# Kernel optimization log

Measured on AMD Instinct MI355X. Metric: run time of the kernel, lower is better.

Reference implementation:

```python
import jax, jax.numpy as jnp
import numpy as np
from jax.scipy.linalg import solve_triangular

REG = 1e-6  # reg_covar added to covariance diagonal
LOG2PI = float(np.log(2.0 * np.pi))
RESP_EPS = 10.0 * float(np.finfo(np.float32).eps)


def _log_gauss(X, means, covs):
    # X: [N,D], means: [K,D], covs: [K,D,D] -> per-sample per-component log N(x|mu_k, Sigma_k): [N,K]
    K, D = means.shape
    eye = jnp.eye(D, dtype=X.dtype)
    chol = jnp.linalg.cholesky(covs + REG * eye)                      # [K,D,D]
    diff = X[None, :, :] - means[:, None, :]                          # [K,N,D]
    sol = jax.vmap(lambda L, d: solve_triangular(L, d.T, lower=True))(chol, diff)  # [K,D,N]
    maha = jnp.sum(sol * sol, axis=1)                                 # [K,N]
    logdet = jnp.sum(jnp.log(jnp.diagonal(chol, axis1=1, axis2=2)), axis=1)  # [K] = 0.5*log|Sigma|
    return (-0.5 * (D * LOG2PI + maha) - logdet[:, None]).T           # [N,K]


def _em_step(X, weights, means, covs):
    N, D = X.shape
    # E-step: responsibilities via stable logsumexp
    lp = _log_gauss(X, means, covs) + jnp.log(weights)[None, :]       # [N,K]
    log_norm = jax.scipy.special.logsumexp(lp, axis=1)                # [N]
    resp = jnp.exp(lp - log_norm[:, None])                            # [N,K]
    # M-step (MLE)
    nk = resp.sum(axis=0) + RESP_EPS                                  # [K]
    new_w = nk / N
    new_means = (resp.T @ X) / nk[:, None]                            # [K,D]
    diff = X[None, :, :] - new_means[:, None, :]                      # [K,N,D]
    new_covs = jnp.einsum('kn,knd,kne->kde', resp.T, diff, diff) / nk[:, None, None]
    new_covs = new_covs + REG * jnp.eye(D, dtype=X.dtype)
    return new_w, new_means, new_covs


def reference(X, weights, means, covariances, n_iter):
    # Normalize provided weights (uniform init in the torch module)
    w0 = weights / jnp.sum(weights)

    def step(carry, _):
        w, m, c = carry
        return _em_step(X, w, m, c), None

    (w, m, c), _ = jax.lax.scan(step, (w0, means, covariances), xs=None, length=n_iter)
    # Final per-sample log-likelihood under the fitted mixture (lower bound)
    lp = _log_gauss(X, m, c) + jnp.log(w)[None, :]
    return jax.scipy.special.logsumexp(lp, axis=1)                    # [N]


def setup_inputs() -> dict:
    key = jax.random.key(0)
    kx, km = jax.random.split(key)
    N, D, K = 100000, 32, 16
    X = jax.random.normal(kx, (N, D), dtype=jnp.float32)
    weights = jnp.ones((K,), dtype=jnp.float32) / K
    means = jax.random.normal(km, (K, D), dtype=jnp.float32)
    covariances = jnp.tile(jnp.eye(D, dtype=jnp.float32)[None], (K, 1, 1))
    return {"X": X, "weights": weights, "means": means, "covariances": covariances, "n_iter": 5}
```

## Files before the change

### kernel.cpp

```cpp
#include <hip/hip_runtime.h>
#include <math.h>

#define REGC 1e-6f
#define LOG2PI 1.83787706640934534f
#define RESP_EPS 1.1920929e-6f

#define PART_K 561
#define RS 16

typedef __attribute__((ext_vector_type(8))) short short8;
typedef __attribute__((ext_vector_type(4))) float f32x4;
typedef unsigned short ushort_t;
typedef unsigned int uint_t;

__device__ __forceinline__ ushort_t f2bf(float x) {
    uint_t u = __float_as_uint(x);
    uint_t r = (u + 0x7fffu + ((u >> 16) & 1u)) >> 16;
    return (ushort_t)r;
}
__device__ __forceinline__ float bf2f(ushort_t h) {
    return __uint_as_float(((uint_t)h) << 16);
}
__device__ __forceinline__ f32x4 shx4(f32x4 v, int m) {
    f32x4 r;
#pragma unroll
    for (int i = 0; i < 4; ++i) r[i] = __shfl_xor(v[i], m);
    return r;
}
__device__ __forceinline__ f32x4 sel4(bool s, f32x4 b, f32x4 a) {
    f32x4 r;
#pragma unroll
    for (int i = 0; i < 4; ++i) r[i] = s ? b[i] : a[i];
    return r;
}
__device__ __forceinline__ short8 pack_rx(const float* r8, const short8 bh, float& row) {
    uint_t u[8];
#pragma unroll
    for (int jj = 0; jj < 8; ++jj) {
        float av = r8[jj] * bf2f((ushort_t)bh[jj]);
        row += av;
        u[jj] = __float_as_uint(av) + 0x8000u;
    }
    short8 out;
    uint_t* o = (uint_t*)&out;
    o[0] = __builtin_amdgcn_perm(u[1], u[0], 0x07060302);
    o[1] = __builtin_amdgcn_perm(u[3], u[2], 0x07060302);
    o[2] = __builtin_amdgcn_perm(u[5], u[4], 0x07060302);
    o[3] = __builtin_amdgcn_perm(u[7], u[6], 0x07060302);
    return out;
}

__global__ __launch_bounds__(256) void gmm_xsplit(const float* __restrict__ X,
                                                  ushort_t* __restrict__ Xh,
                                                  ushort_t* __restrict__ Xl,
                                                  ushort_t* __restrict__ XTH,
                                                  int N) {
    int chunk = blockIdx.x;
    int t = threadIdx.x;
    __shared__ float xsh[32][33];
    int s = t >> 3, q = t & 7;
    int n = chunk * 32 + s;
    float4 v = make_float4(0.f, 0.f, 0.f, 0.f);
    if (n < N) v = ((const float4*)(X + (size_t)n * 32))[q];
    float vv[4] = { v.x, v.y, v.z, v.w };
    xsh[s][q * 4 + 0] = v.x; xsh[s][q * 4 + 1] = v.y;
    xsh[s][q * 4 + 2] = v.z; xsh[s][q * 4 + 3] = v.w;
    if (n < N) {
        ushort_t h[4], l[4];
#pragma unroll
        for (int i = 0; i < 4; ++i) {
            h[i] = f2bf(vv[i]);
            l[i] = f2bf(vv[i] - bf2f(h[i]));
        }
        size_t o = (size_t)n * 32 + q * 4;
        *(uint2*)(Xh + o) = make_uint2((uint_t)h[0] | ((uint_t)h[1] << 16),
                                       (uint_t)h[2] | ((uint_t)h[3] << 16));
        *(uint2*)(Xl + o) = make_uint2((uint_t)l[0] | ((uint_t)l[1] << 16),
                                       (uint_t)l[2] | ((uint_t)l[3] << 16));
    }
    __syncthreads();
    int di = t >> 7;
    int lane = (t >> 1) & 63;
    int jj0 = (t & 1) * 4;
    int c = lane & 15, quad = lane >> 4;
    int d = di * 16 + c;
    ushort_t fh[4];
#pragma unroll
    for (int i = 0; i < 4; ++i) fh[i] = f2bf(xsh[quad * 8 + jj0 + i][d]);
    size_t fo = ((size_t)(chunk * 2 + di) * 64 + lane) * 8 + jj0;
    *(uint2*)(XTH + fo) = make_uint2((uint_t)fh[0] | ((uint_t)fh[1] << 16),
                                     (uint_t)fh[2] | ((uint_t)fh[3] << 16));
}

__global__ __launch_bounds__(64) void gmm_prep0(const float* __restrict__ w,
                                                const float* __restrict__ mu,
                                                const float* __restrict__ cov,
                                                ushort_t* __restrict__ Wh,
                                                ushort_t* __restrict__ Wl,
                                                float* __restrict__ Bv,
                                                float* __restrict__ Cc) {
    int k = blockIdx.x;
    int t = threadIdx.x;
    __shared__ float L[32][33];
    __shared__ float Ai[32][33];
    const float* cv = cov + (size_t)k * 1024;
    const float* muk = mu + (size_t)k * 32;
#pragma unroll
    for (int rep = 0; rep < 16; ++rep) {
        int idx = rep * 64 + t;
        int i = idx >> 5, j = idx & 31;
        L[i][j] = cv[idx] + (i == j ? REGC : 0.f);
    }
    __syncthreads();
#pragma unroll
    for (int j = 0; j < 32; ++j) {
        float s = L[j][j];
#pragma unroll
        for (int p = 0; p < j; ++p) { float v = L[j][p]; s -= v * v; }
        float dj = sqrtf(s);
        if (t > j && t < 32) {
            float s2 = L[t][j];
#pragma unroll
            for (int p = 0; p < j; ++p) s2 -= L[t][p] * L[j][p];
            L[t][j] = s2 / dj;
        }
        if (t == j) L[j][j] = dj;
        __syncthreads();
    }
    if (t < 32) {
        float ai[32];
#pragma unroll
        for (int r = 0; r < 32; ++r) {
            float s = (r == t) ? 1.f : 0.f;
#pragma unroll
            for (int p = 0; p < r; ++p) s -= L[r][p] * ai[p];
            ai[r] = s / L[r][r];
        }
#pragma unroll
        for (int r = 0; r < 32; ++r) Ai[r][t] = ai[r];
    }
    __syncthreads();
#pragma unroll
    for (int rep = 0; rep < 16; ++rep) {
        int idx = rep * 64 + t;
        int i = idx >> 5, j = idx & 31;
        float v = Ai[i][j];
        ushort_t h = f2bf(v);
        Wh[(size_t)(k * 32 + i) * 32 + j] = h;
        Wl[(size_t)(k * 32 + i) * 32 + j] = f2bf(v - bf2f(h));
    }
    if (t < 32) {
        float s = 0.f;
#pragma unroll
        for (int j = 0; j < 32; ++j) s += Ai[t][j] * muk[j];
        Bv[k * 32 + t] = s;
    }
    float wsum = 0.f;
#pragma unroll
    for (int i = 0; i < 16; ++i) wsum += w[i];
    float lv = (t < 32) ? logf(L[t & 31][t & 31]) : 0.f;
#pragma unroll
    for (int off = 1; off < 32; off <<= 1) lv += __shfl_xor(lv, off);
    if (t == 0) Cc[k] = logf(w[k] / wsum) - 0.5f * 32.0f * LOG2PI - lv;
}

__global__ __launch_bounds__(512) __attribute__((amdgpu_waves_per_eu(4)))
void gmm_emstep(const ushort_t* __restrict__ Xh, const ushort_t* __restrict__ Xl,
                const ushort_t* __restrict__ XTH,
                const ushort_t* __restrict__ Wh, const ushort_t* __restrict__ Wl,
                const float* __restrict__ Bv, const float* __restrict__ Cc,
                float* __restrict__ part, int N) {
    __shared__ float rsh[16][260];
    int t = threadIdx.x;
    int wave = t >> 6, lane = t & 63;
    int quad = lane >> 4, c = lane & 15;

    int wstart0 = (int)blockIdx.x * 256 + wave * 32;
    bool dup = (wstart0 + 32 > N);
    int wst = dup ? ((N >= 32) ? N - 32 : 0) : wstart0;

    size_t xo0 = (size_t)(wst + c) * 32 + quad * 8;
    size_t xo1 = (size_t)(wst + 16 + c) * 32 + quad * 8;
    short8 ah0 = *(const short8*)(Xh + xo0);
    short8 al0 = *(const short8*)(Xl + xo0);
    short8 ah1 = *(const short8*)(Xh + xo1);
    short8 al1 = *(const short8*)(Xl + xo1);

    {
        f32x4 p0[2], p1[2], p2[2], p3[2], fin[2];
#pragma unroll
        for (int k = 0; k < 16; ++k) {
            size_t w0 = (size_t)(k * 32 + c) * 32 + quad * 8;
            size_t w1 = w0 + 512;
            short8 bh0 = *(const short8*)(Wh + w0);
            short8 bl0 = *(const short8*)(Wl + w0);
            short8 bh1 = *(const short8*)(Wh + w1);
            short8 bl1 = *(const short8*)(Wl + w1);
            float bv0 = Bv[k * 32 + c];
            float bv1 = Bv[k * 32 + 16 + c];
#pragma unroll
            for (int tt = 0; tt < 2; ++tt) {
                short8 ah = tt ? ah1 : ah0;
                short8 al = tt ? al1 : al0;
                f32x4 a0 = {0.f, 0.f, 0.f, 0.f};
                f32x4 a1 = {0.f, 0.f, 0.f, 0.f};
                a0 = __builtin_amdgcn_mfma_f32_16x16x32_bf16(ah, bh0, a0, 0, 0, 0);
                a0 = __builtin_amdgcn_mfma_f32_16x16x32_bf16(ah, bl0, a0, 0, 0, 0);
                a0 = __builtin_amdgcn_mfma_f32_16x16x32_bf16(al, bh0, a0, 0, 0, 0);
                a1 = __builtin_amdgcn_mfma_f32_16x16x32_bf16(ah, bh1, a1, 0, 0, 0);
                a1 = __builtin_amdgcn_mfma_f32_16x16x32_bf16(ah, bl1, a1, 0, 0, 0);
                a1 = __builtin_amdgcn_mfma_f32_16x16x32_bf16(al, bh1, a1, 0, 0, 0);
                f32x4 ms;
#pragma unroll
                for (int r = 0; r < 4; ++r) {
                    float d0 = a0[r] - bv0;
                    float d1 = a1[r] - bv1;
                    ms[r] = fmaf(d0, d0, d1 * d1);
                }
                if ((k & 1) == 0) { p0[tt] = ms; }
                else {
                    f32x4 a = p0[tt] + shx4(p0[tt], 1);
                    f32x4 b = ms + shx4(ms, 1);
                    f32x4 v = sel4((c & 1) != 0, b, a);
                    if ((k & 2) == 0) { p1[tt] = v; }
                    else {
                        a = p1[tt] + shx4(p1[tt], 2); b = v + shx4(v, 2); v = sel4((c & 2) != 0, b, a);
                        if ((k & 4) == 0) { p2[tt] = v; }
                        else {
                            a = p2[tt] + shx4(p2[tt], 4); b = v + shx4(v, 4); v = sel4((c & 4) != 0, b, a);
                            if ((k & 8) == 0) { p3[tt] = v; }
                            else {
                                a = p3[tt] + shx4(p3[tt], 8); b = v + shx4(v, 8);
                                fin[tt] = sel4((c & 8) != 0, b, a);
                            }
                        }
                    }
                }
            }
        }
        float ccv = Cc[c];
#pragma unroll
        for (int tt = 0; tt < 2; ++tt) {
            f32x4 lp;
#pragma unroll
            for (int r = 0; r < 4; ++r) lp[r] = ccv - 0.5f * fin[tt][r];
            f32x4 mx = lp;
#pragma unroll
            for (int off = 1; off < 16; off <<= 1) {
                f32x4 s = shx4(mx, off);
#pragma unroll
                for (int r = 0; r < 4; ++r) mx[r] = fmaxf(mx[r], s[r]);
            }
            f32x4 e;
#pragma unroll
            for (int r = 0; r < 4; ++r) e[r] = __expf(lp[r] - mx[r]);
            f32x4 sm = e;
#pragma unroll
            for (int off = 1; off < 16; off <<= 1) sm = sm + shx4(sm, off);
            f32x4 sv;
#pragma unroll
            for (int r = 0; r < 4; ++r) sv[r] = dup ? 0.f : e[r] / sm[r];
            *(f32x4*)&rsh[c][wave * 32 + tt * 16 + quad * 4] = sv;
        }
    }
    __syncthreads();

    {
        f32x4 q00[2], q01[2], q11[2];
#pragma unroll
        for (int kk = 0; kk < 2; ++kk) {
            q00[kk] = (f32x4){0.f, 0.f, 0.f, 0.f};
            q01[kk] = (f32x4){0.f, 0.f, 0.f, 0.f};
            q11[kk] = (f32x4){0.f, 0.f, 0.f, 0.f};
        }
        float row0[2] = {0.f, 0.f}, row1[2] = {0.f, 0.f}, corner[2] = {0.f, 0.f};

#pragma unroll 2
        for (int ch = 0; ch < 8; ++ch) {
            size_t fb = (((size_t)((int)blockIdx.x * 8 + ch)) * 128 + lane) * 8;
            short8 bh0 = *(const short8*)(XTH + fb);
            short8 bh1 = *(const short8*)(XTH + fb + 512);
#pragma unroll
            for (int kk = 0; kk < 2; ++kk) {
                int k = wave + kk * 8;
                float r8[8];
#pragma unroll
                for (int jj = 0; jj < 8; ++jj) r8[jj] = rsh[k][ch * 32 + quad * 8 + jj];
                corner[kk] += ((r8[0] + r8[1]) + (r8[2] + r8[3])) +
                              ((r8[4] + r8[5]) + (r8[6] + r8[7]));
                short8 a0 = pack_rx(r8, bh0, row0[kk]);
                short8 a1 = pack_rx(r8, bh1, row1[kk]);
                q00[kk] = __builtin_amdgcn_mfma_f32_16x16x32_bf16(a0, bh0, q00[kk], 0, 0, 0);
                q01[kk] = __builtin_amdgcn_mfma_f32_16x16x32_bf16(a0, bh1, q01[kk], 0, 0, 0);
                q11[kk] = __builtin_amdgcn_mfma_f32_16x16x32_bf16(a1, bh1, q11[kk], 0, 0, 0);
            }
        }
#pragma unroll
        for (int kk = 0; kk < 2; ++kk) {
            row0[kk] += __shfl_xor(row0[kk], 16);  row0[kk] += __shfl_xor(row0[kk], 32);
            row1[kk] += __shfl_xor(row1[kk], 16);  row1[kk] += __shfl_xor(row1[kk], 32);
            corner[kk] += __shfl_xor(corner[kk], 16);  corner[kk] += __shfl_xor(corner[kk], 32);

            int k = wave + kk * 8;
            float* pb = part + ((size_t)blockIdx.x * 16 + k) * PART_K;
#pragma unroll
            for (int r = 0; r < 4; ++r) {
                int i = quad * 4 + r;
                int base = i * 32 - ((i * (i + 1)) >> 1);
                if (c >= i) pb[base + c] = q00[kk][r];
                pb[base + 16 + c] = q01[kk][r];
                int i2 = 16 + i;
                if (c >= i) pb[i2 * 32 - ((i2 * (i2 + 1)) >> 1) + 16 + c] = q11[kk][r];
            }
            if (quad == 0) {
                pb[528 + c] = row0[kk];
                pb[528 + 16 + c] = row1[kk];
            }
            if (lane == 0) pb[560] = corner[kk];
        }
    }
}

__global__ __launch_bounds__(256) void gmm_reduce1(const float* __restrict__ part,
                                                   float* __restrict__ part2,
                                                   int npart) {
    int k = blockIdx.x, g = blockIdx.y;
    int nb = (npart + RS - 1) / RS;
    int b0 = g * nb;
    int b1 = b0 + nb; if (b1 > npart) b1 = npart;
    for (int idx = threadIdx.x; idx < PART_K; idx += 256) {
        float s = 0.f;
#pragma unroll 4
        for (int b = b0; b < b1; ++b)
            s += part[((size_t)b * 16 + k) * PART_K + idx];
        part2[((size_t)g * 16 + k) * PART_K + idx] = s;
    }
}

__global__ __launch_bounds__(256) void gmm_redfin_prep(const float* __restrict__ part2,
                                                       ushort_t* __restrict__ Wh,
                                                       ushort_t* __restrict__ Wl,
                                                       float* __restrict__ Bv,
                                                       float* __restrict__ Cc,
                                                       int N) {
    int k = blockIdx.x;
    int t = threadIdx.x;
    __shared__ float S[561];
    __shared__ float L[1056];
    __shared__ float Ai[1056];
    __shared__ float mean[32];

    for (int idx = t; idx < PART_K; idx += 256) {
        float s = 0.f;
#pragma unroll
        for (int b = 0; b < RS; ++b)
            s += part2[((size_t)b * 16 + k) * PART_K + idx];
        S[idx] = s;
    }
    __syncthreads();
    float nk = S[560] + RESP_EPS;
    float inv = 1.f / nk;
    if (t < 32) mean[t] = S[528 + t] * inv;
    __syncthreads();
#pragma unroll
    for (int i0 = 0; i0 < 4; ++i0) {
        int i = i0 * 8 + (t >> 5), j = t & 31;
        int a = i < j ? i : j;
        int b2 = i < j ? j : i;
        float cv = S[a * 32 - ((a * (a + 1)) >> 1) + b2];
        L[i * 33 + j] = cv * inv - mean[i] * mean[j] + ((i == j) ? 2.f * REGC : 0.f);
    }
    __syncthreads();

#pragma unroll
    for (int j = 0; j < 32; ++j) {
        if (t < 32) {
            float s = L[j * 33 + j];
#pragma unroll
            for (int p = 0; p < j; ++p) { float v = L[j * 33 + p]; s -= v * v; }
            float dj = sqrtf(s);
            if (t > j) {
                float s2 = L[t * 33 + j];
#pragma unroll
                for (int p = 0; p < j; ++p) s2 -= L[t * 33 + p] * L[j * 33 + p];
                L[t * 33 + j] = s2 / dj;
            }
            if (t == j) L[j * 33 + j] = dj;
        }
        __syncthreads();
    }
    if (t < 32) {
        float ai[32];
#pragma unroll
        for (int r = 0; r < 32; ++r) {
            float s = (r == t) ? 1.f : 0.f;
#pragma unroll
            for (int p = 0; p < r; ++p) s -= L[r * 33 + p] * ai[p];
            ai[r] = s / L[r * 33 + r];
        }
#pragma unroll
        for (int r = 0; r < 32; ++r) Ai[r * 33 + t] = ai[r];
    }
    __syncthreads();
#pragma unroll
    for (int i0 = 0; i0 < 4; ++i0) {
        int i = i0 * 8 + (t >> 5), j = t & 31;
        float v = Ai[i * 33 + j];
        ushort_t h = f2bf(v);
        Wh[(size_t)(k * 32 + i) * 32 + j] = h;
        Wl[(size_t)(k * 32 + i) * 32 + j] = f2bf(v - bf2f(h));
    }
    if (t < 32) {
        float s = 0.f;
#pragma unroll
        for (int j = 0; j < 32; ++j) s += Ai[t * 33 + j] * mean[j];
        Bv[k * 32 + t] = s;
    }
    float lv = (t < 32) ? logf(L[(t & 31) * 33 + (t & 31)]) : 0.f;
#pragma unroll
    for (int off = 1; off < 32; off <<= 1) lv += __shfl_xor(lv, off);
    if (t == 0) Cc[k] = logf(nk / (float)N) - 0.5f * 32.0f * LOG2PI - lv;
}

__global__ __launch_bounds__(256, 2) void gmm_estep_fin(const ushort_t* __restrict__ Xh,
                                                        const ushort_t* __restrict__ Xl,
                                                        const ushort_t* __restrict__ Wh,
                                                        const ushort_t* __restrict__ Wl,
                                                        const float* __restrict__ Bv,
                                                        const float* __restrict__ Cc,
                                                        float* __restrict__ out,
                                                        int N) {
    int t = threadIdx.x;
    int wave = t >> 6, lane = t & 63;
    int quad = lane >> 4, c = lane & 15;
    int wstart = (blockIdx.x * 4 + wave) * 32;
    if (wstart + 32 > N) wstart = (N >= 32) ? (N - 32) : 0;
    bool al4 = ((N & 3) == 0);

    size_t xo0 = (size_t)(wstart + c) * 32 + quad * 8;
    size_t xo1 = (size_t)(wstart + 16 + c) * 32 + quad * 8;
    short8 ah0 = *(const short8*)(Xh + xo0);
    short8 al0 = *(const short8*)(Xl + xo0);
    short8 ah1 = *(const short8*)(Xh + xo1);
    short8 al1 = *(const short8*)(Xl + xo1);

    f32x4 p0[2], p1[2], p2[2], p3[2], fin[2];
#pragma unroll
    for (int k = 0; k < 16; ++k) {
        size_t w0 = (size_t)(k * 32 + c) * 32 + quad * 8;
        size_t w1 = w0 + 512;
        short8 bh0 = *(const short8*)(Wh + w0);
        short8 bl0 = *(const short8*)(Wl + w0);
        short8 bh1 = *(const short8*)(Wh + w1);
        short8 bl1 = *(const short8*)(Wl + w1);
        float bv0 = Bv[k * 32 + c];
        float bv1 = Bv[k * 32 + 16 + c];
#pragma unroll
        for (int tt = 0; tt < 2; ++tt) {
            short8 ah = tt ? ah1 : ah0;
            short8 al = tt ? al1 : al0;
            f32x4 a0 = {0.f, 0.f, 0.f, 0.f};
            f32x4 a1 = {0.f, 0.f, 0.f, 0.f};
            a0 = __builtin_amdgcn_mfma_f32_16x16x32_bf16(ah, bh0, a0, 0, 0, 0);
            a0 = __builtin_amdgcn_mfma_f32_16x16x32_bf16(ah, bl0, a0, 0, 0, 0);
            a0 = __builtin_amdgcn_mfma_f32_16x16x32_bf16(al, bh0, a0, 0, 0, 0);
            a1 = __builtin_amdgcn_mfma_f32_16x16x32_bf16(ah, bh1, a1, 0, 0, 0);
            a1 = __builtin_amdgcn_mfma_f32_16x16x32_bf16(ah, bl1, a1, 0, 0, 0);
            a1 = __builtin_amdgcn_mfma_f32_16x16x32_bf16(al, bh1, a1, 0, 0, 0);
            f32x4 ms;
#pragma unroll
            for (int r = 0; r < 4; ++r) {
                float d0 = a0[r] - bv0;
                float d1 = a1[r] - bv1;
                ms[r] = fmaf(d0, d0, d1 * d1);
            }
            if ((k & 1) == 0) { p0[tt] = ms; }
            else {
                f32x4 a = p0[tt] + shx4(p0[tt], 1);
                f32x4 b = ms + shx4(ms, 1);
                f32x4 v = sel4((c & 1) != 0, b, a);
                if ((k & 2) == 0) { p1[tt] = v; }
                else {
                    a = p1[tt] + shx4(p1[tt], 2); b = v + shx4(v, 2); v = sel4((c & 2) != 0, b, a);
                    if ((k & 4) == 0) { p2[tt] = v; }
                    else {
                        a = p2[tt] + shx4(p2[tt], 4); b = v + shx4(v, 4); v = sel4((c & 4) != 0, b, a);
                        if ((k & 8) == 0) { p3[tt] = v; }
                        else {
                            a = p3[tt] + shx4(p3[tt], 8); b = v + shx4(v, 8);
                            fin[tt] = sel4((c & 8) != 0, b, a);
                        }
                    }
                }
            }
        }
    }
    float ccv = Cc[c];
#pragma unroll
    for (int tt = 0; tt < 2; ++tt) {
        f32x4 lp;
#pragma unroll
        for (int r = 0; r < 4; ++r) lp[r] = ccv - 0.5f * fin[tt][r];
        f32x4 mx = lp;
#pragma unroll
        for (int off = 1; off < 16; off <<= 1) {
            f32x4 s = shx4(mx, off);
#pragma unroll
            for (int r = 0; r < 4; ++r) mx[r] = fmaxf(mx[r], s[r]);
        }
        f32x4 e;
#pragma unroll
        for (int r = 0; r < 4; ++r) e[r] = __expf(lp[r] - mx[r]);
        f32x4 sm = e;
#pragma unroll
        for (int off = 1; off < 16; off <<= 1) sm = sm + shx4(sm, off);
        if (c == 0) {
            int nb = wstart + tt * 16 + quad * 4;
            f32x4 o;
#pragma unroll
            for (int r = 0; r < 4; ++r) o[r] = mx[r] + __logf(sm[r]);
            if (al4) *(f32x4*)(out + nb) = o;
            else { for (int r = 0; r < 4; ++r) out[nb + r] = o[r]; }
        }
    }
}

extern "C" void kernel_launch(void* const* d_in, const int* in_sizes, int n_in,
                              void* d_out, int out_size, void* d_ws, size_t ws_size,
                              hipStream_t stream) {
    const float* X   = (const float*)d_in[0];
    const float* w   = (const float*)d_in[1];
    const float* mu  = (const float*)d_in[2];
    const float* cov = (const float*)d_in[3];
    const int NITER = 5;
    int N = in_sizes[0] / 32;
    int MB = (N + 255) / 256;
    int NCB = MB * 8;

    float* ws = (float*)d_ws;
    float*    Bv = ws;
    float*    Cc = ws + 512;
    ushort_t* Wh = (ushort_t*)(ws + 528);
    ushort_t* Wl = (ushort_t*)(ws + 8720);
    ushort_t* Xh = (ushort_t*)(ws + 16912);
    ushort_t* Xl = (ushort_t*)(ws + 16912 + (size_t)16 * N);
    size_t xt0 = 16912 + (size_t)32 * N;
    size_t XTHf = (size_t)NCB * 512;
    ushort_t* XTH = (ushort_t*)(ws + xt0);
    float*  part2 = ws + xt0 + XTHf;
    float*  part  = part2 + (size_t)RS * 16 * PART_K;

    float* out = (float*)d_out;

    int eblocks = ((N + 31) / 32 + 3) / 4;

    gmm_xsplit<<<NCB, 256, 0, stream>>>(X, Xh, Xl, XTH, N);
    gmm_prep0<<<16, 64, 0, stream>>>(w, mu, cov, Wh, Wl, Bv, Cc);

    for (int it = 0; it < NITER; ++it) {
        gmm_emstep<<<MB, 512, 0, stream>>>(Xh, Xl, XTH, Wh, Wl, Bv, Cc, part, N);
        dim3 r1(16, RS);
        gmm_reduce1<<<r1, 256, 0, stream>>>(part, part2, MB);
        gmm_redfin_prep<<<16, 256, 0, stream>>>(part2, Wh, Wl, Bv, Cc, N);
    }
    gmm_estep_fin<<<eblocks, 256, 0, stream>>>(Xh, Xl, Wh, Wl, Bv, Cc, out, N);
}
```

Measured before the change: 454.7 us.

## Replace two-stage partial reduction with global atomics and merge prep kernels

The EM step now accumulates per-component sufficient statistics straight into a single global buffer with atomicAdd, which removes the per-block partial buffer and the separate reduce kernel. The solve kernel reads the sums and zeroes them for the next iteration. The X split and the initial Cholesky prep are fused into one launch, and the single-wave Cholesky drops its block barriers in favour of compiler memory fences. This cuts kernel launches and partial-buffer traffic, at the cost of atomic contention from about 391 blocks hitting the same 16x561 addresses, and non-deterministic float summation order.

```diff
diff --git a/kernel.cpp b/kernel.cpp
--- a/kernel.cpp
+++ b/kernel.cpp
@@ -5,8 +5,7 @@
 #define LOG2PI 1.83787706640934534f
 #define RESP_EPS 1.1920929e-6f
 
-#define PART_K 561
-#define RS 16
+#define SSTR 568
 
 typedef __attribute__((ext_vector_type(8))) short short8;
 typedef __attribute__((ext_vector_type(4))) float f32x4;
@@ -50,59 +49,64 @@
     return out;
 }
 
-__global__ __launch_bounds__(256) void gmm_xsplit(const float* __restrict__ X,
-                                                  ushort_t* __restrict__ Xh,
-                                                  ushort_t* __restrict__ Xl,
-                                                  ushort_t* __restrict__ XTH,
-                                                  int N) {
-    int chunk = blockIdx.x;
-    int t = threadIdx.x;
-    __shared__ float xsh[32][33];
-    int s = t >> 3, q = t & 7;
-    int n = chunk * 32 + s;
-    float4 v = make_float4(0.f, 0.f, 0.f, 0.f);
-    if (n < N) v = ((const float4*)(X + (size_t)n * 32))[q];
-    float vv[4] = { v.x, v.y, v.z, v.w };
-    xsh[s][q * 4 + 0] = v.x; xsh[s][q * 4 + 1] = v.y;
-    xsh[s][q * 4 + 2] = v.z; xsh[s][q * 4 + 3] = v.w;
-    if (n < N) {
-        ushort_t h[4], l[4];
-#pragma unroll
-        for (int i = 0; i < 4; ++i) {
-            h[i] = f2bf(vv[i]);
-            l[i] = f2bf(vv[i] - bf2f(h[i]));
-        }
-        size_t o = (size_t)n * 32 + q * 4;
-        *(uint2*)(Xh + o) = make_uint2((uint_t)h[0] | ((uint_t)h[1] << 16),
-                                       (uint_t)h[2] | ((uint_t)h[3] << 16));
-        *(uint2*)(Xl + o) = make_uint2((uint_t)l[0] | ((uint_t)l[1] << 16),
-                                       (uint_t)l[2] | ((uint_t)l[3] << 16));
-    }
-    __syncthreads();
-    int di = t >> 7;
-    int lane = (t >> 1) & 63;
-    int jj0 = (t & 1) * 4;
-    int c = lane & 15, quad = lane >> 4;
-    int d = di * 16 + c;
-    ushort_t fh[4];
-#pragma unroll
-    for (int i = 0; i < 4; ++i) fh[i] = f2bf(xsh[quad * 8 + jj0 + i][d]);
-    size_t fo = ((size_t)(chunk * 2 + di) * 64 + lane) * 8 + jj0;
-    *(uint2*)(XTH + fo) = make_uint2((uint_t)fh[0] | ((uint_t)fh[1] << 16),
-                                     (uint_t)fh[2] | ((uint_t)fh[3] << 16));
-}
-
-__global__ __launch_bounds__(64) void gmm_prep0(const float* __restrict__ w,
+__global__ __launch_bounds__(256) void gmm_prep(const float* __restrict__ X,
+                                                const float* __restrict__ w,
                                                 const float* __restrict__ mu,
                                                 const float* __restrict__ cov,
+                                                ushort_t* __restrict__ Xh,
+                                                ushort_t* __restrict__ Xl,
+                                                ushort_t* __restrict__ XTH,
                                                 ushort_t* __restrict__ Wh,
                                                 ushort_t* __restrict__ Wl,
                                                 float* __restrict__ Bv,
-                                                float* __restrict__ Cc) {
-    int k = blockIdx.x;
+                                                float* __restrict__ Cc,
+                                                float* __restrict__ S,
+                                                int N, int NCB) {
     int t = threadIdx.x;
+    if ((int)blockIdx.x < NCB) {
+        int chunk = blockIdx.x;
+        __shared__ float xsh[32][33];
+        int s = t >> 3, q = t & 7;
+        int n = chunk * 32 + s;
+        float4 v = make_float4(0.f, 0.f, 0.f, 0.f);
+        if (n < N) v = ((const float4*)(X + (size_t)n * 32))[q];
+        float vv[4] = { v.x, v.y, v.z, v.w };
+        xsh[s][q * 4 + 0] = v.x; xsh[s][q * 4 + 1] = v.y;
+        xsh[s][q * 4 + 2] = v.z; xsh[s][q * 4 + 3] = v.w;
+        if (n < N) {
+            ushort_t h[4], l[4];
+#pragma unroll
+            for (int i = 0; i < 4; ++i) {
+                h[i] = f2bf(vv[i]);
+                l[i] = f2bf(vv[i] - bf2f(h[i]));
+            }
+            size_t o = (size_t)n * 32 + q * 4;
+            *(uint2*)(Xh + o) = make_uint2((uint_t)h[0] | ((uint_t)h[1] << 16),
+                                           (uint_t)h[2] | ((uint_t)h[3] << 16));
+            *(uint2*)(Xl + o) = make_uint2((uint_t)l[0] | ((uint_t)l[1] << 16),
+                                           (uint_t)l[2] | ((uint_t)l[3] << 16));
+        }
+        __syncthreads();
+        int di = t >> 7;
+        int lane = (t >> 1) & 63;
+        int jj0 = (t & 1) * 4;
+        int c = lane & 15, quad = lane >> 4;
+        int d = di * 16 + c;
+        ushort_t fh[4];
+#pragma unroll
+        for (int i = 0; i < 4; ++i) fh[i] = f2bf(xsh[quad * 8 + jj0 + i][d]);
+        size_t fo = ((size_t)(chunk * 2 + di) * 64 + lane) * 8 + jj0;
+        *(uint2*)(XTH + fo) = make_uint2((uint_t)fh[0] | ((uint_t)fh[1] << 16),
+                                         (uint_t)fh[2] | ((uint_t)fh[3] << 16));
+        return;
+    }
+    int k = (int)blockIdx.x - NCB;
     __shared__ float L[32][33];
     __shared__ float Ai[32][33];
+    if (t >= 64) {
+        for (int idx = t - 64; idx < 561; idx += 192) S[(size_t)k * SSTR + idx] = 0.f;
+        return;
+    }
     const float* cv = cov + (size_t)k * 1024;
     const float* muk = mu + (size_t)k * 32;
 #pragma unroll
@@ -111,7 +115,7 @@
         int i = idx >> 5, j = idx & 31;
         L[i][j] = cv[idx] + (i == j ? REGC : 0.f);
     }
-    __syncthreads();
+    asm volatile("" ::: "memory");
 #pragma unroll
     for (int j = 0; j < 32; ++j) {
         float s = L[j][j];
@@ -125,7 +129,7 @@
             L[t][j] = s2 / dj;
         }
         if (t == j) L[j][j] = dj;
-        __syncthreads();
+        asm volatile("" ::: "memory");
     }
     if (t < 32) {
         float ai[32];
@@ -139,7 +143,7 @@
 #pragma unroll
         for (int r = 0; r < 32; ++r) Ai[r][t] = ai[r];
     }
-    __syncthreads();
+    asm volatile("" ::: "memory");
 #pragma unroll
     for (int rep = 0; rep < 16; ++rep) {
         int idx = rep * 64 + t;
@@ -169,7 +173,7 @@
                 const ushort_t* __restrict__ XTH,
                 const ushort_t* __restrict__ Wh, const ushort_t* __restrict__ Wl,
                 const float* __restrict__ Bv, const float* __restrict__ Cc,
-                float* __restrict__ part, int N) {
+                float* __restrict__ S, int N) {
     __shared__ float rsh[16][260];
     int t = threadIdx.x;
     int wave = t >> 6, lane = t & 63;
@@ -302,104 +306,87 @@
             corner[kk] += __shfl_xor(corner[kk], 16);  corner[kk] += __shfl_xor(corner[kk], 32);
 
             int k = wave + kk * 8;
-            float* pb = part + ((size_t)blockIdx.x * 16 + k) * PART_K;
+            float* pb = S + (size_t)k * SSTR;
 #pragma unroll
             for (int r = 0; r < 4; ++r) {
                 int i = quad * 4 + r;
                 int base = i * 32 - ((i * (i + 1)) >> 1);
-                if (c >= i) pb[base + c] = q00[kk][r];
-                pb[base + 16 + c] = q01[kk][r];
+                if (c >= i) atomicAdd(&pb[base + c], q00[kk][r]);
+                atomicAdd(&pb[base + 16 + c], q01[kk][r]);
                 int i2 = 16 + i;
-                if (c >= i) pb[i2 * 32 - ((i2 * (i2 + 1)) >> 1) + 16 + c] = q11[kk][r];
+                if (c >= i) atomicAdd(&pb[i2 * 32 - ((i2 * (i2 + 1)) >> 1) + 16 + c],
+                                      q11[kk][r]);
             }
             if (quad == 0) {
-                pb[528 + c] = row0[kk];
-                pb[528 + 16 + c] = row1[kk];
-            }
-            if (lane == 0) pb[560] = corner[kk];
-        }
-    }
-}
-
-__global__ __launch_bounds__(256) void gmm_reduce1(const float* __restrict__ part,
-                                                   float* __restrict__ part2,
-                                                   int npart) {
-    int k = blockIdx.x, g = blockIdx.y;
-    int nb = (npart + RS - 1) / RS;
-    int b0 = g * nb;
-    int b1 = b0 + nb; if (b1 > npart) b1 = npart;
-    for (int idx = threadIdx.x; idx < PART_K; idx += 256) {
-        float s = 0.f;
-#pragma unroll 4
-        for (int b = b0; b < b1; ++b)
-            s += part[((size_t)b * 16 + k) * PART_K + idx];
-        part2[((size_t)g * 16 + k) * PART_K + idx] = s;
-    }
-}
-
-__global__ __launch_bounds__(256) void gmm_redfin_prep(const float* __restrict__ part2,
-                                                       ushort_t* __restrict__ Wh,
-                                                       ushort_t* __restrict__ Wl,
-                                                       float* __restrict__ Bv,
-                                                       float* __restrict__ Cc,
-                                                       int N) {
+                atomicAdd(&pb[528 + c], row0[kk]);
+                atomicAdd(&pb[528 + 16 + c], row1[kk]);
+            }
+            if (lane == 0) atomicAdd(&pb[560], corner[kk]);
+        }
+    }
+}
+
+__global__ __launch_bounds__(256) void gmm_redsolve(float* __restrict__ S,
+                                                    ushort_t* __restrict__ Wh,
+                                                    ushort_t* __restrict__ Wl,
+                                                    float* __restrict__ Bv,
+                                                    float* __restrict__ Cc,
+                                                    int N) {
     int k = blockIdx.x;
     int t = threadIdx.x;
-    __shared__ float S[561];
+    __shared__ float Ssh[561];
     __shared__ float L[1056];
     __shared__ float Ai[1056];
     __shared__ float mean[32];
 
-    for (int idx = t; idx < PART_K; idx += 256) {
-        float s = 0.f;
-#pragma unroll
-        for (int b = 0; b < RS; ++b)
-            s += part2[((size_t)b * 16 + k) * PART_K + idx];
-        S[idx] = s;
+    for (int idx = t; idx < 561; idx += 256) {
+        float v = S[(size_t)k * SSTR + idx];
+        Ssh[idx] = v;
+        S[(size_t)k * SSTR + idx] = 0.f;
     }
     __syncthreads();
-    float nk = S[560] + RESP_EPS;
+    float nk = Ssh[560] + RESP_EPS;
     float inv = 1.f / nk;
-    if (t < 32) mean[t] = S[528 + t] * inv;
+    if (t < 32) mean[t] = Ssh[528 + t] * inv;
     __syncthreads();
 #pragma unroll
     for (int i0 = 0; i0 < 4; ++i0) {
         int i = i0 * 8 + (t >> 5), j = t & 31;
         int a = i < j ? i : j;
         int b2 = i < j ? j : i;
-        float cv = S[a * 32 - ((a * (a + 1)) >> 1) + b2];
+        float cv = Ssh[a * 32 - ((a * (a + 1)) >> 1) + b2];
         L[i * 33 + j] = cv * inv - mean[i] * mean[j] + ((i == j) ? 2.f * REGC : 0.f);
     }
     __syncthreads();
 
-#pragma unroll
-    for (int j = 0; j < 32; ++j) {
-        if (t < 32) {
+    if (t < 64) {
+#pragma unroll
+        for (int j = 0; j < 32; ++j) {
             float s = L[j * 33 + j];
 #pragma unroll
             for (int p = 0; p < j; ++p) { float v = L[j * 33 + p]; s -= v * v; }
             float dj = sqrtf(s);
-            if (t > j) {
+            if (t > j && t < 32) {
                 float s2 = L[t * 33 + j];
 #pragma unroll
                 for (int p = 0; p < j; ++p) s2 -= L[t * 33 + p] * L[j * 33 + p];
                 L[t * 33 + j] = s2 / dj;
             }
             if (t == j) L[j * 33 + j] = dj;
-        }
-        __syncthreads();
-    }
-    if (t < 32) {
-        float ai[32];
-#pragma unroll
-        for (int r = 0; r < 32; ++r) {
-            float s = (r == t) ? 1.f : 0.f;
-#pragma unroll
-            for (int p = 0; p < r; ++p) s -= L[r * 33 + p] * ai[p];
-            ai[r] = s / L[r * 33 + r];
-        }
-#pragma unroll
-        for (int r = 0; r < 32; ++r) Ai[r * 33 + t] = ai[r];
+            asm volatile("" ::: "memory");
+        }
+        if (t < 32) {
+            float ai[32];
+#pragma unroll
+            for (int r = 0; r < 32; ++r) {
+                float s = (r == t) ? 1.f : 0.f;
+#pragma unroll
+                for (int p = 0; p < r; ++p) s -= L[r * 33 + p] * ai[p];
+                ai[r] = s / L[r * 33 + r];
+            }
+#pragma unroll
+            for (int r = 0; r < 32; ++r) Ai[r * 33 + t] = ai[r];
+        }
     }
     __syncthreads();
 #pragma unroll
@@ -547,21 +534,18 @@
     size_t xt0 = 16912 + (size_t)32 * N;
     size_t XTHf = (size_t)NCB * 512;
     ushort_t* XTH = (ushort_t*)(ws + xt0);
-    float*  part2 = ws + xt0 + XTHf;
-    float*  part  = part2 + (size_t)RS * 16 * PART_K;
+    float*  S   = ws + xt0 + XTHf;
 
     float* out = (float*)d_out;
 
     int eblocks = ((N + 31) / 32 + 3) / 4;
 
-    gmm_xsplit<<<NCB, 256, 0, stream>>>(X, Xh, Xl, XTH, N);
-    gmm_prep0<<<16, 64, 0, stream>>>(w, mu, cov, Wh, Wl, Bv, Cc);
+    gmm_prep<<<NCB + 16, 256, 0, stream>>>(X, w, mu, cov, Xh, Xl, XTH, Wh, Wl,
+                                           Bv, Cc, S, N, NCB);
 
     for (int it = 0; it < NITER; ++it) {
-        gmm_emstep<<<MB, 512, 0, stream>>>(Xh, Xl, XTH, Wh, Wl, Bv, Cc, part, N);
-        dim3 r1(16, RS);
-        gmm_reduce1<<<r1, 256, 0, stream>>>(part, part2, MB);
-        gmm_redfin_prep<<<16, 256, 0, stream>>>(part2, Wh, Wl, Bv, Cc, N);
+        gmm_emstep<<<MB, 512, 0, stream>>>(Xh, Xl, XTH, Wh, Wl, Bv, Cc, S, N);
+        gmm_redsolve<<<16, 256, 0, stream>>>(S, Wh, Wl, Bv, Cc, N);
     }
     gmm_estep_fin<<<eblocks, 256, 0, stream>>>(Xh, Xl, Wh, Wl, Bv, Cc, out, N);
 }
```

New measurement: 641.6 us. +41.1%, slower.
